# Optimization experiments

Hardware: AMD Instinct MI355X
Metric: run time of the kernel (lower is better)

Reference implementation:

```python
import jax, jax.numpy as jnp
import numpy as np

N_CODES, N_EDGES, EMB, N_C, NNZ = 4096, 8192, 128, 4, 65536
ADD_RATIO, TEMP = 0.1, 0.5
MASK_VAL = -1e9


def setup_inputs() -> dict:
    key = jax.random.key(0)
    k1, k2, k3, k4, k5 = jax.random.split(key, 5)
    X = jax.random.normal(k1, (N_CODES, EMB), jnp.float32)
    V = jax.random.randint(k2, (NNZ,), 0, N_CODES)
    E = jax.random.randint(k3, (NNZ,), 0, N_EDGES)
    # incidence matrix has 1s exactly at the (V, E) nonzero entries
    H = jnp.zeros((N_CODES, N_EDGES), jnp.float32).at[V, E].set(1.0)
    p = jnp.clip(jax.random.uniform(k4, (N_CODES, N_EDGES), jnp.float32), 0.05, 0.95)
    cos_weight = jax.random.normal(k5, (N_C, EMB), jnp.float32)
    return {"X": X, "H": H, "V": V, "E": E,
            "incident_mask_prob": p, "cos_weight": cos_weight}


def _l2norm(x):
    # F.normalize(x, p=2, dim=-1, eps=1e-6): x / max(||x||, eps)
    n = jnp.sqrt(jnp.sum(x * x, axis=-1, keepdims=True))
    return x / jnp.maximum(n, 1e-6)


def reference(X, H, V, E, incident_mask_prob, cos_weight):
    num_edges = H.shape[1]
    n_c = cos_weight.shape[0]
    # 1) edge embeddings: scatter-mean of incident code embeddings
    sums = jax.ops.segment_sum(X[V], E, num_segments=num_edges)      # (M, D)
    cnt = jax.ops.segment_sum(jnp.ones((V.shape[0],), X.dtype), E,
                              num_segments=num_edges)                 # (M,)
    eX = sums / jnp.maximum(cnt, 1.0)[:, None]
    # 2) multi-head cosine similarity, mean over heads
    node_m = _l2norm(X[:, None, :] * cos_weight[None])               # (N, h, D)
    edge_m = _l2norm(eX[:, None, :] * cos_weight[None])              # (M, h, D)
    S = jnp.einsum('nhd,mhd->nm', node_m, edge_m) / n_c              # (N, M)
    # mask out existing incidences
    S = S.at[V, E].set(MASK_VAL)
    # 3) global top-k new incidences (k is static)
    k = int(ADD_RATIO * V.shape[0])
    _, idx = jax.lax.top_k(S.reshape(-1), k)
    row = idx // num_edges
    col = idx % num_edges
    delta_H = jnp.zeros_like(H).at[row, col].set(1.0)
    enriched_H = H + delta_H
    # 4) RelaxedBernoulli(temperature, probs).rsample()
    u = jax.random.uniform(jax.random.key(42), H.shape, H.dtype,
                           minval=1e-6, maxval=1.0 - 1e-6)
    logits = (jnp.log(incident_mask_prob) - jnp.log1p(-incident_mask_prob)
              + jnp.log(u) - jnp.log1p(-u)) / TEMP
    incident_mask = jax.nn.sigmoid(logits)
    return enriched_H * incident_mask
```

## Files before the change

### kernel.cpp

```cpp
#include <hip/hip_runtime.h>
#include <math.h>

#define N_CODES 4096
#define N_EDGES 8192
#define EMB     128
#define NHEAD   4
#define NNZ     65536
#define K_TOP   6553
#define K_SAMP  820
#define S_TOTAL 33554432
#define NBINS   8192
#define NREP    16
#define CAP2    131072
#define SLACK_BINS 14
#define TIE_CAP 1024
#define LBUF    4096
#define SAMP_ITEMS (S_TOTAL / 8 / 8)

typedef _Float16 f16_t;
typedef __attribute__((ext_vector_type(8))) _Float16 f16x8;
typedef __attribute__((ext_vector_type(4))) float f32x4;

__device__ __forceinline__ unsigned rotl32(unsigned v, int r) {
  return (v << r) | (v >> (32 - r));
}

__device__ float jax_u42(unsigned pos) {
  const unsigned ks0 = 0u, ks1 = 42u, ks2 = 0x1BD11BDAu ^ 0u ^ 42u;
  unsigned x0 = 0u  + ks0;
  unsigned x1 = pos + ks1;
#define TFR(r) { x0 += x1; x1 = rotl32(x1, (r)); x1 ^= x0; }
  TFR(13) TFR(15) TFR(26) TFR(6)   x0 += ks1; x1 += ks2 + 1u;
  TFR(17) TFR(29) TFR(16) TFR(24)  x0 += ks2; x1 += ks0 + 2u;
  TFR(13) TFR(15) TFR(26) TFR(6)   x0 += ks0; x1 += ks1 + 3u;
  TFR(17) TFR(29) TFR(16) TFR(24)  x0 += ks1; x1 += ks2 + 4u;
  TFR(13) TFR(15) TFR(26) TFR(6)   x0 += ks2; x1 += ks0 + 5u;
#undef TFR
  unsigned bits = x0 ^ x1;
  unsigned fb = (bits >> 9) | 0x3f800000u;
  float f = __uint_as_float(fb) - 1.0f;
  const float minv = 1e-6f;
  const float maxv = (float)(1.0 - 1e-6);
  float u = f * (maxv - minv) + minv;
  return fmaxf(minv, u);
}

__device__ float mask_val(float p, unsigned pos) {
  float u = jax_u42(pos);
  float l = (logf(p) - log1pf(-p) + logf(u) - log1pf(-u)) * 2.0f;
  return 1.0f / (1.0f + expf(-l));
}

__device__ __forceinline__ unsigned long long f64key(double v) {
  long long b = __double_as_longlong(v);
  return (b < 0) ? ~(unsigned long long)b
                 : ((unsigned long long)b | 0x8000000000000000ULL);
}

__global__ void count_k(const int* __restrict__ E, int* __restrict__ cnt) {
  int i = blockIdx.x * blockDim.x + threadIdx.x;
  if (i < NNZ) atomicAdd(&cnt[E[i]], 1);
}

__global__ __launch_bounds__(1024) void scan_k(const int* __restrict__ cnt,
                                               int* __restrict__ offs) {
  __shared__ int part[1024];
  int t = threadIdx.x;
  int local[8]; int s = 0;
  for (int j = 0; j < 8; ++j) { local[j] = cnt[t * 8 + j]; s += local[j]; }
  part[t] = s; __syncthreads();
  int v = s;
  for (int o = 1; o < 1024; o <<= 1) {
    int add = (t >= o) ? part[t - o] : 0;
    __syncthreads();
    v += add; part[t] = v;
    __syncthreads();
  }
  int base = v - s;
  for (int j = 0; j < 8; ++j) { offs[t * 8 + j] = base; base += local[j]; }
}

__global__ void scatter_k(const int* __restrict__ E, const int* __restrict__ offs,
                          int* __restrict__ cursor, int* __restrict__ bucket) {
  int i = blockIdx.x * blockDim.x + threadIdx.x;
  if (i < NNZ) {
    int e = E[i];
    int p = atomicAdd(&cursor[e], 1);
    bucket[offs[e] + p] = i;
  }
}

__global__ __launch_bounds__(128) void edge_k(const float* __restrict__ X,
                                              const int* __restrict__ V,
                                              const int* __restrict__ cnt,
                                              const int* __restrict__ offs,
                                              int* __restrict__ bucket,
                                              const float* __restrict__ W,
                                              f16_t* __restrict__ B16) {
  __shared__ int lst[512];
  __shared__ float red[2];
  int m = blockIdx.x, t = threadIdx.x;
  int deg = cnt[m], off = offs[m];
  int n = min(deg, 512);
  for (int j = t; j < n; j += 128) lst[j] = bucket[off + j];
  __syncthreads();
  if (t == 0 && n > 1) {
    for (int a = 1; a < n; ++a) {
      int key = lst[a]; int b = a - 1;
      while (b >= 0 && lst[b] > key) { lst[b + 1] = lst[b]; --b; }
      lst[b + 1] = key;
    }
  }
  __syncthreads();
  for (int j = t; j < n; j += 128) bucket[off + j] = lst[j];
  float s = 0.f;
  for (int j = 0; j < n; ++j) s += X[(size_t)V[lst[j]] * EMB + t];
  float eXd = s / fmaxf((float)deg, 1.0f);
  int lane = t & 63, wv = t >> 6;
  for (int h = 0; h < NHEAD; ++h) {
    float wd = W[h * EMB + t];
    float val = eXd * wd;
    float ss = val * val;
    for (int o = 32; o > 0; o >>= 1) ss += __shfl_down(ss, o, 64);
    if (lane == 0) red[wv] = ss;
    __syncthreads();
    float nh = 1.0f / fmaxf(sqrtf(red[0] + red[1]), 1e-6f);
    B16[(size_t)m * (NHEAD * EMB) + h * EMB + t] = (f16_t)(eXd * wd * wd * nh);
    __syncthreads();
  }
}

__global__ __launch_bounds__(128) void node_k(const float* __restrict__ X,
                                              const float* __restrict__ W,
                                              f16_t* __restrict__ A16) {
  __shared__ float red[2];
  int nid = blockIdx.x, t = threadIdx.x;
  float xd = X[(size_t)nid * EMB + t];
  int lane = t & 63, wv = t >> 6;
  for (int h = 0; h < NHEAD; ++h) {
    float val = xd * W[h * EMB + t];
    float ss = val * val;
    for (int o = 32; o > 0; o >>= 1) ss += __shfl_down(ss, o, 64);
    if (lane == 0) red[wv] = ss;
    __syncthreads();
    float nh = 1.0f / fmaxf(sqrtf(red[0] + red[1]), 1e-6f);
    A16[(size_t)nid * (NHEAD * EMB) + h * EMB + t] = (f16_t)(xd * nh);
    __syncthreads();
  }
}

__global__ __launch_bounds__(256) void gemm_k(const f16_t* __restrict__ A16,
                                              const f16_t* __restrict__ B16,
                                              unsigned short* __restrict__ S16) {
  __shared__ __align__(16) f16_t As[128 * 32];
  __shared__ __align__(16) f16_t Bs[128 * 32];
  const int tid  = threadIdx.x;
  const int lane = tid & 63;
  const int wv   = tid >> 6;
  const int m0   = blockIdx.x * 128;
  const int n0   = blockIdx.y * 128;
  const int wr   = (wv >> 1) * 64;
  const int wc   = (wv & 1) * 64;
  const int frow = lane & 15;
  const int fg   = lane >> 4;
  const int sw   = (frow >> 1) & 3;
  const int fo   = ((fg ^ sw) << 3);

  f32x4 acc[4][4];
#pragma unroll
  for (int i = 0; i < 4; ++i)
#pragma unroll
    for (int j = 0; j < 4; ++j) acc[i][j] = (f32x4){0.f, 0.f, 0.f, 0.f};

  for (int k0 = 0; k0 < 512; k0 += 32) {
    __syncthreads();
#pragma unroll
    for (int r = 0; r < 2; ++r) {
      int chunk = r * 256 + wv * 64 + lane;
      int row   = chunk >> 2;
      int cb    = ((chunk & 3) ^ ((chunk >> 3) & 3)) << 3;
      __builtin_amdgcn_global_load_lds(
          (const __attribute__((address_space(1))) void*)
              (A16 + ((size_t)(n0 + row) << 9) + k0 + cb),
          (__attribute__((address_space(3))) void*)
              (As + (size_t)(r * 256 + wv * 64) * 8),
          16, 0, 0);
      __builtin_amdgcn_global_load_lds(
          (const __attribute__((address_space(1))) void*)
              (B16 + ((size_t)(m0 + row) << 9) + k0 + cb),
          (__attribute__((address_space(3))) void*)
              (Bs + (size_t)(r * 256 + wv * 64) * 8),
          16, 0, 0);
    }
    __syncthreads();
    f16x8 a[4], b[4];
#pragma unroll
    for (int i = 0; i < 4; ++i)
      a[i] = *(const f16x8*)(As + (wr + i * 16 + frow) * 32 + fo);
#pragma unroll
    for (int j = 0; j < 4; ++j)
      b[j] = *(const f16x8*)(Bs + (wc + j * 16 + frow) * 32 + fo);
#pragma unroll
    for (int i = 0; i < 4; ++i)
#pragma unroll
      for (int j = 0; j < 4; ++j)
        acc[i][j] = __builtin_amdgcn_mfma_f32_16x16x32_f16(a[i], b[j], acc[i][j], 0, 0, 0);
  }
#pragma unroll
  for (int i = 0; i < 4; ++i)
#pragma unroll
    for (int q = 0; q < 4; ++q) {
      int row = n0 + wr + i * 16 + fg * 4 + q;
      unsigned short* Sr = S16 + (size_t)row * N_EDGES + m0 + wc;
#pragma unroll
      for (int j = 0; j < 4; ++j) {
        f16_t h = (f16_t)(acc[i][j][q] * 0.25f);
        Sr[j * 16 + frow] = __builtin_bit_cast(unsigned short, h);
      }
    }
}

__global__ void maskset16_k(const int* __restrict__ V, const int* __restrict__ E,
                            unsigned short* __restrict__ S16) {
  int i = blockIdx.x * blockDim.x + threadIdx.x;
  if (i < NNZ) S16[(size_t)V[i] * N_EDGES + E[i]] = 0xFC00u;
}

__global__ __launch_bounds__(256) void hist16_k(const f16x8* __restrict__ S8,
                                                unsigned* __restrict__ ghist) {
  __shared__ unsigned hh[NBINS];
  for (int i = threadIdx.x; i < NBINS; i += 256) hh[i] = 0;
  __syncthreads();
  const int stride = gridDim.x * blockDim.x;
  int j = blockIdx.x * blockDim.x + threadIdx.x;
#define BIN8(v)                                                              \
  _Pragma("unroll") for (int c = 0; c < 8; ++c) {                            \
    float bf = fminf(fmaxf(((float)(v)[c] + 1.0f) * 4096.0f, 0.0f),          \
                     (float)(NBINS - 1));                                    \
    atomicAdd(&hh[(int)bf], 1u);                                             \
  }
#define SIDX(jj) (((jj) >> 6) * 512 + ((jj) & 63))
  for (; j + 3 * stride < SAMP_ITEMS; j += 4 * stride) {
    f16x8 v0 = S8[SIDX(j)];
    f16x8 v1 = S8[SIDX(j + stride)];
    f16x8 v2 = S8[SIDX(j + 2 * stride)];
    f16x8 v3 = S8[SIDX(j + 3 * stride)];
    BIN8(v0) BIN8(v1) BIN8(v2) BIN8(v3)
  }
  for (; j < SAMP_ITEMS; j += stride) { f16x8 v = S8[SIDX(j)]; BIN8(v) }
#undef SIDX
#undef BIN8
  __syncthreads();
  unsigned* gh = ghist + (size_t)(blockIdx.x & (NREP - 1)) * NBINS;
  for (int i2 = threadIdx.x; i2 < NBINS; i2 += 256) {
    unsigned c = hh[i2];
    if (c) atomicAdd(&gh[i2], c);
  }
}

__global__ __launch_bounds__(1024) void thresh_k(const unsigned* __restrict__ hist,
                                                 float* __restrict__ T_lo) {
  __shared__ int suff[1024];
  int t = threadIdx.x;
  const int G = NBINS / 1024;
  int b0 = t * G;
  int s = 0;
  for (int j = 0; j < G; ++j) {
    unsigned tb = 0;
    for (int r = 0; r < NREP; ++r) tb += hist[(size_t)r * NBINS + b0 + j];
    s += (int)tb;
  }
  int v = s;
  suff[t] = v; __syncthreads();
  for (int o = 1; o < 1024; o <<= 1) {
    int add = (t + o < 1024) ? suff[t + o] : 0;
    __syncthreads();
    v += add; suff[t] = v;
    __syncthreads();
  }
  int above = (t < 1023) ? suff[t + 1] : 0;
  if (above < K_SAMP && suff[t] >= K_SAMP) {
    int running = above;
    int B = b0;
    for (int b = b0 + G - 1; b >= b0; --b) {
      unsigned tb = 0;
      for (int r = 0; r < NREP; ++r) tb += hist[(size_t)r * NBINS + b];
      running += (int)tb;
      if (running >= K_SAMP) { B = b; break; }
    }
    B = max(B, SLACK_BINS);
    *T_lo = (float)(B - SLACK_BINS) * (1.0f / 4096.0f) - 1.0f;
  }
}

__global__ __launch_bounds__(256) void collect16_k(const f16x8* __restrict__ S8,
                                                   const float* __restrict__ T_lo_p,
                                                   unsigned* __restrict__ counter,
                                                   int* __restrict__ ci) {
  __shared__ int lbuf[LBUF];
  __shared__ unsigned lcnt, gbase;
  if (threadIdx.x == 0) lcnt = 0;
  __syncthreads();
  float T = *T_lo_p;
  const int stride = gridDim.x * blockDim.x;
  int i = blockIdx.x * blockDim.x + threadIdx.x;
#define SEL8(v, base)                                                        \
  _Pragma("unroll") for (int c = 0; c < 8; ++c) {                            \
    if ((float)(v)[c] >= T) {                                                \
      unsigned j = atomicAdd(&lcnt, 1u);                                     \
      if (j < LBUF) lbuf[j] = (base) * 8 + c;                                \
      else { unsigned g = atomicAdd(counter, 1u);                            \
             if (g < CAP2) ci[g] = (base) * 8 + c; }                         \
    }                                                                        \
  }
  for (; i + 3 * stride < S_TOTAL / 8; i += 4 * stride) {
    f16x8 v0 = S8[i];
    f16x8 v1 = S8[i + stride];
    f16x8 v2 = S8[i + 2 * stride];
    f16x8 v3 = S8[i + 3 * stride];
    SEL8(v0, i) SEL8(v1, i + stride) SEL8(v2, i + 2 * stride) SEL8(v3, i + 3 * stride)
  }
  for (; i < S_TOTAL / 8; i += stride) { f16x8 v = S8[i]; SEL8(v, i) }
#undef SEL8
  __syncthreads();
  unsigned n = min(lcnt, (unsigned)LBUF);
  if (threadIdx.x == 0) gbase = atomicAdd(counter, n);
  __syncthreads();
  unsigned gb = gbase;
  for (unsigned t = threadIdx.x; t < n; t += 256) {
    unsigned p = gb + t;
    if (p < CAP2) ci[p] = lbuf[t];
  }
}

__global__ __launch_bounds__(256) void rescore_k(const float* __restrict__ X,
                                                 const float* __restrict__ W,
                                                 const int* __restrict__ V,
                                                 const int* __restrict__ cnt,
                                                 const int* __restrict__ offs,
                                                 const int* __restrict__ bucket,
                                                 const int* __restrict__ ci,
                                                 const unsigned* __restrict__ counter,
                                                 unsigned long long* __restrict__ ckey) {
  int C = (int)min(*counter, (unsigned)CAP2);
  int wave = threadIdx.x >> 6, lane = threadIdx.x & 63;
  int j = blockIdx.x * 4 + wave;
  if (j >= C) return;
  int pos = ci[j];
  int n = pos >> 13;
  int m = pos & 8191;
  int deg = cnt[m], off = offs[m];
  int nmem = min(deg, 512);
  double e0 = 0.0, e1 = 0.0;
  for (int q = 0; q < nmem; ++q) {
    const float* xv = X + (size_t)V[bucket[off + q]] * EMB;
    e0 += (double)xv[lane];
    e1 += (double)xv[lane + 64];
  }
  double dd = fmax((double)deg, 1.0);
  e0 /= dd; e1 /= dd;
  const float* xr = X + (size_t)n * EMB;
  double x0 = (double)xr[lane], x1 = (double)xr[lane + 64];
  double s = 0.0;
  for (int h = 0; h < NHEAD; ++h) {
    const float* wr = W + h * EMB;
    double w0 = (double)wr[lane], w1 = (double)wr[lane + 64];
    double xw0 = x0 * w0, xw1 = x1 * w1;
    double ew0 = e0 * w0, ew1 = e1 * w1;
    double an = xw0 * xw0 + xw1 * xw1;
    double ae = ew0 * ew0 + ew1 * ew1;
    double dt = xw0 * ew0 + xw1 * ew1;
    for (int o = 32; o > 0; o >>= 1) {
      an += __shfl_down(an, o, 64);
      ae += __shfl_down(ae, o, 64);
      dt += __shfl_down(dt, o, 64);
    }
    if (lane == 0) {
      double Nn = fmax(sqrt(an), 1e-6);
      double Ne = fmax(sqrt(ae), 1e-6);
      s += dt / (Nn * Ne);
    }
  }
  if (lane == 0) ckey[j] = f64key(s * 0.25);
}

__global__ __launch_bounds__(1024) void kth_k(const unsigned long long* __restrict__ keys,
                                              const unsigned* __restrict__ counter,
                                              unsigned long long* __restrict__ thr) {
  __shared__ unsigned hist[256];
  __shared__ unsigned long long s_prefix;
  __shared__ unsigned s_kleft, s_cgreat;
  int C = (int)min(*counter, (unsigned)CAP2);
  if (threadIdx.x == 0) { s_prefix = 0ULL; s_kleft = K_TOP; s_cgreat = 0u; }
  __syncthreads();
  for (int level = 7; level >= 0; --level) {
    for (int i = threadIdx.x; i < 256; i += 1024) hist[i] = 0;
    __syncthreads();
    unsigned long long prefix = s_prefix;
    unsigned long long pmask = (level == 7) ? 0ULL : (~0ULL << ((level + 1) * 8));
    for (int i = threadIdx.x; i < C; i += 1024) {
      unsigned long long k = keys[i];
      if ((k & pmask) == prefix)
        atomicAdd(&hist[(unsigned)((k >> (level * 8)) & 0xFF)], 1u);
    }
    __syncthreads();
    if (threadIdx.x == 0) {
      unsigned cum = 0; int b = 0;
      for (int i = 255; i >= 0; --i) {
        if (cum + hist[i] >= s_kleft) { b = i; break; }
        cum += hist[i];
      }
      s_prefix |= ((unsigned long long)b << (level * 8));
      s_kleft  -= cum;
      s_cgreat += cum;
    }
    __syncthreads();
  }
  if (threadIdx.x == 0) { thr[0] = s_prefix; thr[1] = (unsigned long long)s_cgreat; }
}

__global__ void write_k(const unsigned long long* __restrict__ keys,
                        const int* __restrict__ ci,
                        const unsigned* __restrict__ counter,
                        const unsigned long long* __restrict__ thr,
                        const float* __restrict__ P, float* __restrict__ out,
                        int* __restrict__ tiebuf, unsigned* __restrict__ tiecnt) {
  int C = (int)min(*counter, (unsigned)CAP2);
  int j = blockIdx.x * blockDim.x + threadIdx.x;
  if (j >= C) return;
  unsigned long long k = keys[j];
  unsigned long long t = thr[0];
  if (k > t) {
    unsigned pos = (unsigned)ci[j];
    out[pos] = mask_val(P[pos], pos);
  } else if (k == t) {
    unsigned q = atomicAdd(tiecnt, 1u);
    if (q < TIE_CAP) tiebuf[q] = ci[j];
  }
}

__global__ __launch_bounds__(256) void tiefin_k(const int* __restrict__ tiebuf,
                                                const unsigned* __restrict__ tiecnt,
                                                const unsigned long long* __restrict__ thr,
                                                const float* __restrict__ P,
                                                float* __restrict__ out) {
  __shared__ int idx[TIE_CAP];
  int T = (int)min(*tiecnt, (unsigned)TIE_CAP);
  int need = K_TOP - (int)thr[1];
  if (need <= 0 || T == 0) return;
  for (int i = threadIdx.x; i < T; i += 256) idx[i] = tiebuf[i];
  __syncthreads();
  if (threadIdx.x == 0 && T > 1) {
    for (int a = 1; a < T; ++a) {
      int key = idx[a]; int b = a - 1;
      while (b >= 0 && idx[b] > key) { idx[b + 1] = idx[b]; --b; }
      idx[b + 1] = key;
    }
  }
  __syncthreads();
  int m = min(need, T);
  for (int i = threadIdx.x; i < m; i += 256) {
    unsigned pos = (unsigned)idx[i];
    out[pos] = mask_val(P[pos], pos);
  }
}

__global__ void scatterH_k(const int* __restrict__ V, const int* __restrict__ E,
                           const float* __restrict__ P, float* __restrict__ out) {
  int i = blockIdx.x * blockDim.x + threadIdx.x;
  if (i >= NNZ) return;
  unsigned pos = (unsigned)V[i] * (unsigned)N_EDGES + (unsigned)E[i];
  out[pos] = mask_val(P[pos], pos);
}

extern "C" void kernel_launch(void* const* d_in, const int* in_sizes, int n_in,
                              void* d_out, int out_size, void* d_ws, size_t ws_size,
                              hipStream_t stream) {
  const float* X = (const float*)d_in[0];
  const int*   V = (const int*)d_in[2];
  const int*   E = (const int*)d_in[3];
  const float* P = (const float*)d_in[4];
  const float* W = (const float*)d_in[5];
  float* OUT = (float*)d_out;

  unsigned short* S16 = (unsigned short*)((char*)d_out + (size_t)S_TOTAL * 2);

  char* w = (char*)d_ws;
  int*      cnt      = (int*)(w + 0);
  int*      offs     = (int*)(w + 32768);
  int*      cursor   = (int*)(w + 65536);
  int*      bucket   = (int*)(w + 98304);
  unsigned* counter  = (unsigned*)(w + 360448);
  float*    T_lo     = (float*)(w + 360452);
  unsigned* tiecnt   = (unsigned*)(w + 360456);
  unsigned long long* thr = (unsigned long long*)(w + 360464);
  int*      cand_idx = (int*)(w + 360704);
  unsigned* ghist    = (unsigned*)(w + 360704);
  unsigned long long* cand_key = (unsigned long long*)(w + 884992);
  int*      tiebuf   = (int*)(w + 1933568);
  f16_t*    A16      = (f16_t*)(w + 1937664);
  f16_t*    B16      = (f16_t*)(w + 6131968);

  hipMemsetAsync(cnt,     0, 32768, stream);
  hipMemsetAsync(cursor,  0, 32768, stream);
  hipMemsetAsync((void*)(w + 360448), 0, 64, stream);
  hipMemsetAsync(ghist,   0, (size_t)NREP * NBINS * 4, stream);

  count_k     <<<NNZ / 256, 256, 0, stream>>>(E, cnt);
  scan_k      <<<1, 1024, 0, stream>>>(cnt, offs);
  scatter_k   <<<NNZ / 256, 256, 0, stream>>>(E, offs, cursor, bucket);
  edge_k      <<<N_EDGES, 128, 0, stream>>>(X, V, cnt, offs, bucket, W, B16);
  node_k      <<<N_CODES, 128, 0, stream>>>(X, W, A16);
  gemm_k      <<<dim3(N_EDGES / 128, N_CODES / 128), 256, 0, stream>>>(A16, B16, S16);
  maskset16_k <<<NNZ / 256, 256, 0, stream>>>(V, E, S16);
  hist16_k    <<<256, 256, 0, stream>>>((const f16x8*)S16, ghist);
  thresh_k    <<<1, 1024, 0, stream>>>(ghist, T_lo);
  collect16_k <<<1024, 256, 0, stream>>>((const f16x8*)S16, T_lo, counter, cand_idx);
  rescore_k   <<<CAP2 / 4, 256, 0, stream>>>(X, W, V, cnt, offs, bucket,
                                             cand_idx, counter, cand_key);
  kth_k       <<<1, 1024, 0, stream>>>(cand_key, counter, thr);
  hipMemsetAsync(d_out, 0, (size_t)S_TOTAL * 4, stream);
  write_k     <<<CAP2 / 256, 256, 0, stream>>>(cand_key, cand_idx, counter, thr,
                                               P, OUT, tiebuf, tiecnt);
  tiefin_k    <<<1, 256, 0, stream>>>(tiebuf, tiecnt, thr, P, OUT);
  scatterH_k  <<<NNZ / 256, 256, 0, stream>>>(V, E, P, OUT);
}
```

Baseline: 501.1 us.

## Fuse prep kernels, stage GEMM epilogue in LDS, cache edge means for rescore

Merges the edge and node normalization kernels into one launch and merges the candidate write and incidence scatter kernels. The edge kernel now also writes double-precision edge means, so rescore reads them instead of re-gathering member rows per candidate. The GEMM epilogue stages the output tile in shared memory and writes coalesced 8-byte rows. Other changes: kth histogram loop unrolled, collect grid doubled, and the memsets collapsed into one. This trades an extra global buffer and an LDS round-trip for fewer launches and less redundant gather work.

```diff
diff --git a/kernel.cpp b/kernel.cpp
--- a/kernel.cpp
+++ b/kernel.cpp
@@ -16,6 +16,7 @@
 #define TIE_CAP 1024
 #define LBUF    4096
 #define SAMP_ITEMS (S_TOTAL / 8 / 8)
+#define WBLK    (CAP2 / 256)
 
 typedef _Float16 f16_t;
 typedef __attribute__((ext_vector_type(8))) _Float16 f16x8;
@@ -90,70 +91,76 @@
   }
 }
 
-__global__ __launch_bounds__(128) void edge_k(const float* __restrict__ X,
+__global__ __launch_bounds__(128) void prep_k(const float* __restrict__ X,
                                               const int* __restrict__ V,
                                               const int* __restrict__ cnt,
                                               const int* __restrict__ offs,
-                                              int* __restrict__ bucket,
+                                              const int* __restrict__ bucket,
                                               const float* __restrict__ W,
-                                              f16_t* __restrict__ B16) {
+                                              f16_t* __restrict__ A16,
+                                              f16_t* __restrict__ B16,
+                                              double* __restrict__ eX64) {
   __shared__ int lst[512];
   __shared__ float red[2];
-  int m = blockIdx.x, t = threadIdx.x;
-  int deg = cnt[m], off = offs[m];
-  int n = min(deg, 512);
-  for (int j = t; j < n; j += 128) lst[j] = bucket[off + j];
-  __syncthreads();
-  if (t == 0 && n > 1) {
-    for (int a = 1; a < n; ++a) {
-      int key = lst[a]; int b = a - 1;
-      while (b >= 0 && lst[b] > key) { lst[b + 1] = lst[b]; --b; }
-      lst[b + 1] = key;
-    }
-  }
-  __syncthreads();
-  for (int j = t; j < n; j += 128) bucket[off + j] = lst[j];
-  float s = 0.f;
-  for (int j = 0; j < n; ++j) s += X[(size_t)V[lst[j]] * EMB + t];
-  float eXd = s / fmaxf((float)deg, 1.0f);
+  int bid = blockIdx.x, t = threadIdx.x;
   int lane = t & 63, wv = t >> 6;
-  for (int h = 0; h < NHEAD; ++h) {
-    float wd = W[h * EMB + t];
-    float val = eXd * wd;
-    float ss = val * val;
-    for (int o = 32; o > 0; o >>= 1) ss += __shfl_down(ss, o, 64);
-    if (lane == 0) red[wv] = ss;
-    __syncthreads();
-    float nh = 1.0f / fmaxf(sqrtf(red[0] + red[1]), 1e-6f);
-    B16[(size_t)m * (NHEAD * EMB) + h * EMB + t] = (f16_t)(eXd * wd * wd * nh);
-    __syncthreads();
-  }
-}
-
-__global__ __launch_bounds__(128) void node_k(const float* __restrict__ X,
-                                              const float* __restrict__ W,
-                                              f16_t* __restrict__ A16) {
-  __shared__ float red[2];
-  int nid = blockIdx.x, t = threadIdx.x;
-  float xd = X[(size_t)nid * EMB + t];
-  int lane = t & 63, wv = t >> 6;
-  for (int h = 0; h < NHEAD; ++h) {
-    float val = xd * W[h * EMB + t];
-    float ss = val * val;
-    for (int o = 32; o > 0; o >>= 1) ss += __shfl_down(ss, o, 64);
-    if (lane == 0) red[wv] = ss;
-    __syncthreads();
-    float nh = 1.0f / fmaxf(sqrtf(red[0] + red[1]), 1e-6f);
-    A16[(size_t)nid * (NHEAD * EMB) + h * EMB + t] = (f16_t)(xd * nh);
-    __syncthreads();
+  if (bid < N_EDGES) {
+    int m = bid;
+    int deg = cnt[m], off = offs[m];
+    int n = min(deg, 512);
+    for (int j = t; j < n; j += 128) lst[j] = bucket[off + j];
+    __syncthreads();
+    if (t == 0 && n > 1) {
+      for (int a = 1; a < n; ++a) {
+        int key = lst[a]; int b = a - 1;
+        while (b >= 0 && lst[b] > key) { lst[b + 1] = lst[b]; --b; }
+        lst[b + 1] = key;
+      }
+    }
+    __syncthreads();
+    float s = 0.f;
+    double s64 = 0.0;
+    for (int j = 0; j < n; ++j) {
+      float xv = X[(size_t)V[lst[j]] * EMB + t];
+      s += xv;
+      s64 += (double)xv;
+    }
+    float eXd = s / fmaxf((float)deg, 1.0f);
+    eX64[(size_t)m * EMB + t] = s64 / fmax((double)deg, 1.0);
+    for (int h = 0; h < NHEAD; ++h) {
+      float wd = W[h * EMB + t];
+      float val = eXd * wd;
+      float ss = val * val;
+      for (int o = 32; o > 0; o >>= 1) ss += __shfl_down(ss, o, 64);
+      if (lane == 0) red[wv] = ss;
+      __syncthreads();
+      float nh = 1.0f / fmaxf(sqrtf(red[0] + red[1]), 1e-6f);
+      B16[(size_t)m * (NHEAD * EMB) + h * EMB + t] = (f16_t)(eXd * wd * wd * nh);
+      __syncthreads();
+    }
+  } else {
+    int nid = bid - N_EDGES;
+    float xd = X[(size_t)nid * EMB + t];
+    for (int h = 0; h < NHEAD; ++h) {
+      float val = xd * W[h * EMB + t];
+      float ss = val * val;
+      for (int o = 32; o > 0; o >>= 1) ss += __shfl_down(ss, o, 64);
+      if (lane == 0) red[wv] = ss;
+      __syncthreads();
+      float nh = 1.0f / fmaxf(sqrtf(red[0] + red[1]), 1e-6f);
+      A16[(size_t)nid * (NHEAD * EMB) + h * EMB + t] = (f16_t)(xd * nh);
+      __syncthreads();
+    }
   }
 }
 
 __global__ __launch_bounds__(256) void gemm_k(const f16_t* __restrict__ A16,
                                               const f16_t* __restrict__ B16,
                                               unsigned short* __restrict__ S16) {
-  __shared__ __align__(16) f16_t As[128 * 32];
-  __shared__ __align__(16) f16_t Bs[128 * 32];
+  __shared__ __align__(16) unsigned char smem[128 * 132 * 2];
+  f16_t* As = (f16_t*)smem;
+  f16_t* Bs = (f16_t*)(smem + 8192);
+  unsigned short* Cs = (unsigned short*)smem;
   const int tid  = threadIdx.x;
   const int lane = tid & 63;
   const int wv   = tid >> 6;
@@ -206,18 +213,25 @@
       for (int j = 0; j < 4; ++j)
         acc[i][j] = __builtin_amdgcn_mfma_f32_16x16x32_f16(a[i], b[j], acc[i][j], 0, 0, 0);
   }
+  __syncthreads();
 #pragma unroll
   for (int i = 0; i < 4; ++i)
 #pragma unroll
-    for (int q = 0; q < 4; ++q) {
-      int row = n0 + wr + i * 16 + fg * 4 + q;
-      unsigned short* Sr = S16 + (size_t)row * N_EDGES + m0 + wc;
-#pragma unroll
-      for (int j = 0; j < 4; ++j) {
+    for (int j = 0; j < 4; ++j)
+#pragma unroll
+      for (int q = 0; q < 4; ++q) {
+        int rl = wr + i * 16 + fg * 4 + q;
+        int cl = wc + j * 16 + frow;
         f16_t h = (f16_t)(acc[i][j][q] * 0.25f);
-        Sr[j * 16 + frow] = __builtin_bit_cast(unsigned short, h);
+        Cs[rl * 132 + cl] = __builtin_bit_cast(unsigned short, h);
       }
-    }
+  __syncthreads();
+  for (int idx = tid; idx < 128 * 32; idx += 256) {
+    int r  = idx >> 5;
+    int ch = idx & 31;
+    *(unsigned long long*)(S16 + (size_t)(n0 + r) * N_EDGES + m0 + ch * 4) =
+        *(const unsigned long long*)(Cs + r * 132 + ch * 4);
+  }
 }
 
 __global__ void maskset16_k(const int* __restrict__ V, const int* __restrict__ E,
@@ -335,10 +349,7 @@
 
 __global__ __launch_bounds__(256) void rescore_k(const float* __restrict__ X,
                                                  const float* __restrict__ W,
-                                                 const int* __restrict__ V,
-                                                 const int* __restrict__ cnt,
-                                                 const int* __restrict__ offs,
-                                                 const int* __restrict__ bucket,
+                                                 const double* __restrict__ eX64,
                                                  const int* __restrict__ ci,
                                                  const unsigned* __restrict__ counter,
                                                  unsigned long long* __restrict__ ckey) {
@@ -349,16 +360,8 @@
   int pos = ci[j];
   int n = pos >> 13;
   int m = pos & 8191;
-  int deg = cnt[m], off = offs[m];
-  int nmem = min(deg, 512);
-  double e0 = 0.0, e1 = 0.0;
-  for (int q = 0; q < nmem; ++q) {
-    const float* xv = X + (size_t)V[bucket[off + q]] * EMB;
-    e0 += (double)xv[lane];
-    e1 += (double)xv[lane + 64];
-  }
-  double dd = fmax((double)deg, 1.0);
-  e0 /= dd; e1 /= dd;
+  double e0 = eX64[(size_t)m * EMB + lane];
+  double e1 = eX64[(size_t)m * EMB + lane + 64];
   const float* xr = X + (size_t)n * EMB;
   double x0 = (double)xr[lane], x1 = (double)xr[lane + 64];
   double s = 0.0;
@@ -398,19 +401,30 @@
     __syncthreads();
     unsigned long long prefix = s_prefix;
     unsigned long long pmask = (level == 7) ? 0ULL : (~0ULL << ((level + 1) * 8));
-    for (int i = threadIdx.x; i < C; i += 1024) {
+    int sh = level * 8;
+    int i = threadIdx.x;
+    for (; i + 3 * 1024 < C; i += 4 * 1024) {
+      unsigned long long k0 = keys[i];
+      unsigned long long k1 = keys[i + 1024];
+      unsigned long long k2 = keys[i + 2048];
+      unsigned long long k3 = keys[i + 3072];
+      if ((k0 & pmask) == prefix) atomicAdd(&hist[(unsigned)((k0 >> sh) & 0xFF)], 1u);
+      if ((k1 & pmask) == prefix) atomicAdd(&hist[(unsigned)((k1 >> sh) & 0xFF)], 1u);
+      if ((k2 & pmask) == prefix) atomicAdd(&hist[(unsigned)((k2 >> sh) & 0xFF)], 1u);
+      if ((k3 & pmask) == prefix) atomicAdd(&hist[(unsigned)((k3 >> sh) & 0xFF)], 1u);
+    }
+    for (; i < C; i += 1024) {
       unsigned long long k = keys[i];
-      if ((k & pmask) == prefix)
-        atomicAdd(&hist[(unsigned)((k >> (level * 8)) & 0xFF)], 1u);
+      if ((k & pmask) == prefix) atomicAdd(&hist[(unsigned)((k >> sh) & 0xFF)], 1u);
     }
     __syncthreads();
     if (threadIdx.x == 0) {
       unsigned cum = 0; int b = 0;
-      for (int i = 255; i >= 0; --i) {
-        if (cum + hist[i] >= s_kleft) { b = i; break; }
-        cum += hist[i];
+      for (int i2 = 255; i2 >= 0; --i2) {
+        if (cum + hist[i2] >= s_kleft) { b = i2; break; }
+        cum += hist[i2];
       }
-      s_prefix |= ((unsigned long long)b << (level * 8));
+      s_prefix |= ((unsigned long long)b << sh);
       s_kleft  -= cum;
       s_cgreat += cum;
     }
@@ -419,23 +433,32 @@
   if (threadIdx.x == 0) { thr[0] = s_prefix; thr[1] = (unsigned long long)s_cgreat; }
 }
 
-__global__ void write_k(const unsigned long long* __restrict__ keys,
-                        const int* __restrict__ ci,
-                        const unsigned* __restrict__ counter,
-                        const unsigned long long* __restrict__ thr,
-                        const float* __restrict__ P, float* __restrict__ out,
-                        int* __restrict__ tiebuf, unsigned* __restrict__ tiecnt) {
-  int C = (int)min(*counter, (unsigned)CAP2);
-  int j = blockIdx.x * blockDim.x + threadIdx.x;
-  if (j >= C) return;
-  unsigned long long k = keys[j];
-  unsigned long long t = thr[0];
-  if (k > t) {
-    unsigned pos = (unsigned)ci[j];
+__global__ void wsH_k(const unsigned long long* __restrict__ keys,
+                      const int* __restrict__ ci,
+                      const unsigned* __restrict__ counter,
+                      const unsigned long long* __restrict__ thr,
+                      const float* __restrict__ P, float* __restrict__ out,
+                      int* __restrict__ tiebuf, unsigned* __restrict__ tiecnt,
+                      const int* __restrict__ V, const int* __restrict__ E) {
+  int b = blockIdx.x;
+  if (b < WBLK) {
+    int C = (int)min(*counter, (unsigned)CAP2);
+    int j = b * 256 + threadIdx.x;
+    if (j >= C) return;
+    unsigned long long k = keys[j];
+    unsigned long long t = thr[0];
+    if (k > t) {
+      unsigned pos = (unsigned)ci[j];
+      out[pos] = mask_val(P[pos], pos);
+    } else if (k == t) {
+      unsigned q = atomicAdd(tiecnt, 1u);
+      if (q < TIE_CAP) tiebuf[q] = ci[j];
+    }
+  } else {
+    int i = (b - WBLK) * 256 + threadIdx.x;
+    if (i >= NNZ) return;
+    unsigned pos = (unsigned)V[i] * (unsigned)N_EDGES + (unsigned)E[i];
     out[pos] = mask_val(P[pos], pos);
-  } else if (k == t) {
-    unsigned q = atomicAdd(tiecnt, 1u);
-    if (q < TIE_CAP) tiebuf[q] = ci[j];
   }
 }
 
@@ -465,14 +488,6 @@
   }
 }
 
-__global__ void scatterH_k(const int* __restrict__ V, const int* __restrict__ E,
-                           const float* __restrict__ P, float* __restrict__ out) {
-  int i = blockIdx.x * blockDim.x + threadIdx.x;
-  if (i >= NNZ) return;
-  unsigned pos = (unsigned)V[i] * (unsigned)N_EDGES + (unsigned)E[i];
-  out[pos] = mask_val(P[pos], pos);
-}
-
 extern "C" void kernel_launch(void* const* d_in, const int* in_sizes, int n_in,
                               void* d_out, int out_size, void* d_ws, size_t ws_size,
                               hipStream_t stream) {
@@ -487,41 +502,37 @@
 
   char* w = (char*)d_ws;
   int*      cnt      = (int*)(w + 0);
-  int*      offs     = (int*)(w + 32768);
-  int*      cursor   = (int*)(w + 65536);
-  int*      bucket   = (int*)(w + 98304);
-  unsigned* counter  = (unsigned*)(w + 360448);
-  float*    T_lo     = (float*)(w + 360452);
-  unsigned* tiecnt   = (unsigned*)(w + 360456);
-  unsigned long long* thr = (unsigned long long*)(w + 360464);
-  int*      cand_idx = (int*)(w + 360704);
-  unsigned* ghist    = (unsigned*)(w + 360704);
-  unsigned long long* cand_key = (unsigned long long*)(w + 884992);
-  int*      tiebuf   = (int*)(w + 1933568);
-  f16_t*    A16      = (f16_t*)(w + 1937664);
-  f16_t*    B16      = (f16_t*)(w + 6131968);
-
-  hipMemsetAsync(cnt,     0, 32768, stream);
-  hipMemsetAsync(cursor,  0, 32768, stream);
-  hipMemsetAsync((void*)(w + 360448), 0, 64, stream);
-  hipMemsetAsync(ghist,   0, (size_t)NREP * NBINS * 4, stream);
+  int*      cursor   = (int*)(w + 32768);
+  unsigned* counter  = (unsigned*)(w + 65536);
+  float*    T_lo     = (float*)(w + 65540);
+  unsigned* tiecnt   = (unsigned*)(w + 65544);
+  unsigned long long* thr = (unsigned long long*)(w + 65552);
+  unsigned* ghist    = (unsigned*)(w + 65792);
+  int*      offs     = (int*)(w + 590080);
+  int*      bucket   = (int*)(w + 622848);
+  int*      cand_idx = (int*)(w + 884992);
+  unsigned long long* cand_key = (unsigned long long*)(w + 1409280);
+  int*      tiebuf   = (int*)(w + 2457856);
+  f16_t*    A16      = (f16_t*)(w + 2461952);
+  f16_t*    B16      = (f16_t*)(w + 6656256);
+  double*   eX64     = (double*)(w + 15044864);
+
+  hipMemsetAsync(w, 0, 590080, stream);
 
   count_k     <<<NNZ / 256, 256, 0, stream>>>(E, cnt);
   scan_k      <<<1, 1024, 0, stream>>>(cnt, offs);
   scatter_k   <<<NNZ / 256, 256, 0, stream>>>(E, offs, cursor, bucket);
-  edge_k      <<<N_EDGES, 128, 0, stream>>>(X, V, cnt, offs, bucket, W, B16);
-  node_k      <<<N_CODES, 128, 0, stream>>>(X, W, A16);
+  prep_k      <<<N_EDGES + N_CODES, 128, 0, stream>>>(X, V, cnt, offs, bucket, W,
+                                                      A16, B16, eX64);
   gemm_k      <<<dim3(N_EDGES / 128, N_CODES / 128), 256, 0, stream>>>(A16, B16, S16);
   maskset16_k <<<NNZ / 256, 256, 0, stream>>>(V, E, S16);
   hist16_k    <<<256, 256, 0, stream>>>((const f16x8*)S16, ghist);
   thresh_k    <<<1, 1024, 0, stream>>>(ghist, T_lo);
-  collect16_k <<<1024, 256, 0, stream>>>((const f16x8*)S16, T_lo, counter, cand_idx);
-  rescore_k   <<<CAP2 / 4, 256, 0, stream>>>(X, W, V, cnt, offs, bucket,
-                                             cand_idx, counter, cand_key);
+  collect16_k <<<2048, 256, 0, stream>>>((const f16x8*)S16, T_lo, counter, cand_idx);
+  rescore_k   <<<CAP2 / 4, 256, 0, stream>>>(X, W, eX64, cand_idx, counter, cand_key);
   kth_k       <<<1, 1024, 0, stream>>>(cand_key, counter, thr);
   hipMemsetAsync(d_out, 0, (size_t)S_TOTAL * 4, stream);
-  write_k     <<<CAP2 / 256, 256, 0, stream>>>(cand_key, cand_idx, counter, thr,
-                                               P, OUT, tiebuf, tiecnt);
+  wsH_k       <<<WBLK + NNZ / 256, 256, 0, stream>>>(cand_key, cand_idx, counter, thr,
+                                                     P, OUT, tiebuf, tiecnt, V, E);
   tiefin_k    <<<1, 256, 0, stream>>>(tiebuf, tiecnt, thr, P, OUT);
-  scatterH_k  <<<NNZ / 256, 256, 0, stream>>>(V, E, P, OUT);
-}
+}
```

New measurement: 497.7 us, median of 2. About the same (-0.7%).
